# Kernel optimization log

Measured on AMD Instinct MI355X. Metric: run time of the kernel, lower is better.

Reference implementation:

```python
import jax, jax.numpy as jnp
import numpy as np

B, C, H, W = 8, 256, 128, 128
KC, VC, HEADS = 256, 256, 8


def setup_inputs() -> dict:
    key = jax.random.key(0)
    ks = jax.random.split(key, 10)
    s = 0.05
    return {
        "x": jax.random.normal(ks[0], (B, C, H, W), jnp.float32),
        "Wk": jax.random.normal(ks[1], (KC, C), jnp.float32) * s,
        "bk": jax.random.normal(ks[2], (KC,), jnp.float32) * s,
        "Wq": jax.random.normal(ks[3], (KC, C), jnp.float32) * s,
        "bq": jax.random.normal(ks[4], (KC,), jnp.float32) * s,
        "Wv": jax.random.normal(ks[5], (VC, C), jnp.float32) * s,
        "bv": jax.random.normal(ks[6], (VC,), jnp.float32) * s,
        "Wr": jax.random.normal(ks[7], (C, VC), jnp.float32) * s,
        "br": jax.random.normal(ks[8], (C,), jnp.float32) * s,
        "head_count": HEADS,
    }


def reference(x, Wk, bk, Wq, bq, Wv, bv, Wr, br, head_count):
    n, c, h, w = x.shape
    hw = h * w
    xf = x.reshape(n, c, hw)  # [n, C, S]
    # 1x1 convs == per-pixel linear projections
    keys = jnp.einsum('kc,ncs->nks', Wk, xf) + bk[None, :, None]
    queries = jnp.einsum('kc,ncs->nks', Wq, xf) + bq[None, :, None]
    values = jnp.einsum('vc,ncs->nvs', Wv, xf) + bv[None, :, None]

    dk = Wk.shape[0] // head_count
    dv = Wv.shape[0] // head_count
    # split heads along channel dim (matches torch channel slicing)
    K = jax.nn.softmax(keys.reshape(n, head_count, dk, hw), axis=-1)   # softmax over spatial
    Q = jax.nn.softmax(queries.reshape(n, head_count, dk, hw), axis=2) # softmax over key dim
    V = values.reshape(n, head_count, dv, hw)

    # context = K @ V^T : [n, h, dk, dv]
    ctx = jnp.einsum('nhks,nhvs->nhkv', K, V)
    # attended = ctx^T @ Q : [n, h, dv, S]
    att = jnp.einsum('nhkv,nhks->nhvs', ctx, Q).reshape(n, head_count * dv, h, w)

    attention = jnp.einsum('ov,nvhw->nohw', Wr, att) + br[None, :, None, None]
    # attention map: per-head mean over key dim, then mean over heads
    attention_map = K.mean(axis=2).mean(axis=1).reshape(n, h, w)
    # torch returns the LAST head's context (loop variable after the loop)
    context_last = ctx[:, -1]
    return attention, context_last, attention_map
```

## Files before the change

kernel.cpp:

```cpp
#include <hip/hip_runtime.h>
#include <hip/hip_bf16.h>

typedef float f32x4 __attribute__((ext_vector_type(4)));
typedef short s16x8 __attribute__((ext_vector_type(8)));
typedef __bf16 bf16x8 __attribute__((ext_vector_type(8)));
typedef unsigned short u16;

#define DEVI __device__ __forceinline__

static constexpr int    HW      = 16384;
static constexpr size_t BSTRIDE = (size_t)256 * HW;

static constexpr size_t oXBT   = 0;
static constexpr size_t oEK    = oXBT  + (size_t)8 * HW * 256 * 2;
static constexpr size_t oQT    = oEK   + (size_t)8 * 256 * HW * 2;
static constexpr size_t oVB    = oQT   + (size_t)8 * HW * 256 * 2;
static constexpr size_t oWK    = oVB   + (size_t)8 * 256 * HW * 2;
static constexpr size_t oBIAS  = oWK   + (size_t)768 * 256 * 2;
static constexpr size_t oISE   = oBIAS + 4096;
static constexpr size_t oPS    = oISE  + 8192;
static constexpr size_t oCTX   = oPS   + (size_t)256 * 2048 * 4;
static constexpr size_t oMB    = oCTX  + (size_t)64 * 1024 * 4;
static constexpr size_t oCPART = oMB   + (size_t)8 * 256 * 256 * 2;
static constexpr size_t oMPART = oCPART + (size_t)4096 * 1024 * 4;

DEVI float bf2f(short x) {
  unsigned u = ((unsigned)(unsigned short)x) << 16;
  return __builtin_bit_cast(float, u);
}
DEVI u16 f2bf(float x) { return __builtin_bit_cast(u16, (__bf16)x); }

DEVI void gld16(const void* g, void* l) {
  __builtin_amdgcn_global_load_lds(
      (__attribute__((address_space(1))) void*)(g),
      (__attribute__((address_space(3))) void*)(l), 16, 0, 0);
}

__global__ __launch_bounds__(256) void k_prep(
    const float* __restrict__ Wk, const float* __restrict__ Wq, const float* __restrict__ Wv,
    const float* __restrict__ bk, const float* __restrict__ bq, const float* __restrict__ bv,
    u16* __restrict__ Wkqv, float* __restrict__ bias)
{
  int i = blockIdx.x * 256 + threadIdx.x;
  for (int p = i; p < 768 * 256; p += 64 * 256) {
    float v = (p < 65536) ? Wk[p] : (p < 131072 ? Wq[p - 65536] : Wv[p - 131072]);
    Wkqv[p] = f2bf(v);
  }
  if (i < 768) bias[i] = (i < 256) ? bk[i] : (i < 512 ? bq[i - 256] : bv[i - 512]);
}

__global__ __launch_bounds__(256) void k_transpose(const float* __restrict__ in_, u16* __restrict__ out)
{
  __shared__ u16 lds[64 * 256];
  const int t = threadIdx.x;
  const int n = blockIdx.y;
  const int s0 = blockIdx.x * 64;
  const float* src = in_ + ((size_t)n * 256 + t) * HW + s0;
  #pragma unroll
  for (int i = 0; i < 16; ++i) {
    f32x4 v = *(const f32x4*)(src + i * 4);
    #pragma unroll
    for (int j = 0; j < 4; ++j) lds[(i * 4 + j) * 256 + t] = f2bf(v[j]);
  }
  __syncthreads();
  s16x8* gp = (s16x8*)(out + (size_t)n * BSTRIDE + (size_t)s0 * 256);
  const s16x8* lp = (const s16x8*)lds;
  #pragma unroll
  for (int i = 0; i < 8; ++i) gp[t + i * 256] = lp[t + i * 256];
}

__global__ __launch_bounds__(256) void k_proj(
    const u16* __restrict__ W, const u16* __restrict__ xbT, const float* __restrict__ bias,
    u16* __restrict__ ek, u16* __restrict__ qT, u16* __restrict__ vb, float* __restrict__ ps)
{
  __shared__ u16 smem[17408];
  u16* Al = smem;
  u16* Bl = smem + 8192;
  const int t = threadIdx.x;
  const int L = blockIdx.x;
  const int n  = L & 7;
  const int idx = L >> 3;
  const int mb = idx % 6;
  const int sb = idx / 6;
  const int m0 = mb * 128, s0 = sb * 128;
  const int lane = t & 63;
  const int l15 = lane & 15, l4 = lane >> 4;
  const int wv = t >> 6;
  const int wm = (wv & 1) * 64, wn = (wv >> 1) * 64;
  const u16* Ab = W + (size_t)m0 * 256;
  const u16* Bb = xbT + (size_t)n * BSTRIDE + (size_t)s0 * 256;
  const int ar = t >> 2, ac = (t & 3) * 8;

  f32x4 acc[4][4] = {};

  auto stage = [&](int buf, int k0) {
    gld16(Ab + (size_t)ar * 256 + k0 + ac,        Al + buf * 4096 + t * 8);
    gld16(Ab + (size_t)(ar + 64) * 256 + k0 + ac, Al + buf * 4096 + 2048 + t * 8);
    gld16(Bb + (size_t)ar * 256 + k0 + ac,        Bl + buf * 4096 + t * 8);
    gld16(Bb + (size_t)(ar + 64) * 256 + k0 + ac, Bl + buf * 4096 + 2048 + t * 8);
  };

  stage(0, 0);
  __syncthreads();
  #pragma unroll
  for (int kt = 0; kt < 8; ++kt) {
    const int buf = kt & 1;
    if (kt < 7) stage(buf ^ 1, (kt + 1) * 32);
    bf16x8 af[4], bff[4];
    #pragma unroll
    for (int g = 0; g < 4; ++g) {
      af[g]  = *(const bf16x8*)&Al[buf * 4096 + (wm + g * 16 + l15) * 32 + l4 * 8];
      bff[g] = *(const bf16x8*)&Bl[buf * 4096 + (wn + g * 16 + l15) * 32 + l4 * 8];
    }
    #pragma unroll
    for (int mg = 0; mg < 4; ++mg)
      #pragma unroll
      for (int ng = 0; ng < 4; ++ng)
        acc[mg][ng] = __builtin_amdgcn_mfma_f32_16x16x32_bf16(af[mg], bff[ng], acc[mg][ng], 0, 0, 0);
    __syncthreads();
  }

  #pragma unroll
  for (int mg = 0; mg < 4; ++mg)
    #pragma unroll
    for (int r = 0; r < 4; ++r) {
      const float bb = bias[m0 + wm + mg * 16 + l4 * 4 + r];
      #pragma unroll
      for (int ng = 0; ng < 4; ++ng) acc[mg][ng][r] += bb;
    }

  const int rowBase = (mb & 1) * 128;

  if (mb < 2) {
    #pragma unroll
    for (int mg = 0; mg < 4; ++mg)
      #pragma unroll
      for (int r = 0; r < 4; ++r) {
        float s_ = 0.f;
        #pragma unroll
        for (int ng = 0; ng < 4; ++ng) {
          const float e = __expf(acc[mg][ng][r]);
          acc[mg][ng][r] = e; s_ += e;
        }
        s_ += __shfl_xor(s_, 1); s_ += __shfl_xor(s_, 2);
        s_ += __shfl_xor(s_, 4); s_ += __shfl_xor(s_, 8);
        if (l15 == 0) {
          const int row = rowBase + wm + mg * 16 + l4 * 4 + r;
          ps[((size_t)(sb * 2 + (wn >> 6))) * 2048 + n * 256 + row] = s_;
        }
      }
    u16* O = ek + (size_t)n * BSTRIDE;
    #pragma unroll
    for (int mg = 0; mg < 4; ++mg)
      #pragma unroll
      for (int r = 0; r < 4; ++r) {
        const size_t row = rowBase + wm + mg * 16 + l4 * 4 + r;
        u16* op = O + row * HW + s0 + wn + l15;
        #pragma unroll
        for (int ng = 0; ng < 4; ++ng) op[ng * 16] = f2bf(acc[mg][ng][r]);
      }
  } else if (mb < 4) {
    #pragma unroll
    for (int hh = 0; hh < 2; ++hh)
      #pragma unroll
      for (int ng = 0; ng < 4; ++ng) {
        float s = 0.f;
        #pragma unroll
        for (int mg = hh * 2; mg < hh * 2 + 2; ++mg)
          #pragma unroll
          for (int r = 0; r < 4; ++r) { const float e = __expf(acc[mg][ng][r]); acc[mg][ng][r] = e; s += e; }
        s += __shfl_xor(s, 16);
        s += __shfl_xor(s, 32);
        const float inv = 1.f / s;
        #pragma unroll
        for (int mg = hh * 2; mg < hh * 2 + 2; ++mg)
          #pragma unroll
          for (int r = 0; r < 4; ++r) acc[mg][ng][r] *= inv;
      }
    #pragma unroll
    for (int mg = 0; mg < 4; ++mg)
      #pragma unroll
      for (int ng = 0; ng < 4; ++ng)
        #pragma unroll
        for (int r = 0; r < 4; ++r) {
          const int srow = wn + ng * 16 + l15;
          const int mcol = wm + mg * 16 + l4 * 4 + r;
          smem[srow * 136 + mcol] = f2bf(acc[mg][ng][r]);
        }
    __syncthreads();
    u16* O = qT + (size_t)n * BSTRIDE + (size_t)s0 * 256 + rowBase;
    #pragma unroll
    for (int it = 0; it < 8; ++it) {
      const int row = it * 16 + (t >> 4);
      *(s16x8*)(O + (size_t)row * 256 + (t & 15) * 8) = *(const s16x8*)&smem[row * 136 + (t & 15) * 8];
    }
  } else {
    u16* O = vb + (size_t)n * BSTRIDE;
    #pragma unroll
    for (int mg = 0; mg < 4; ++mg)
      #pragma unroll
      for (int r = 0; r < 4; ++r) {
        const size_t row = rowBase + wm + mg * 16 + l4 * 4 + r;
        u16* op = O + row * HW + s0 + wn + l15;
        #pragma unroll
        for (int ng = 0; ng < 4; ++ng) op[ng * 16] = f2bf(acc[mg][ng][r]);
      }
  }
}

__global__ __launch_bounds__(256) void k_inv(const float* __restrict__ ps, float* __restrict__ ise)
{
  const int i = blockIdx.x * 256 + threadIdx.x;
  float s = 0.f;
  for (int b = 0; b < 256; ++b) s += ps[(size_t)b * 2048 + i];
  ise[i] = 1.f / s;
}

__global__ __launch_bounds__(64) void k_ctx_part(
    const u16* __restrict__ ek, const u16* __restrict__ vb, const float* __restrict__ ise,
    float* __restrict__ cpart, float* __restrict__ mpart)
{
  const int blk = blockIdx.x;
  const int chunk = blk & 63, nh = blk >> 6;
  const int h = nh & 7, n = nh >> 3;
  const int lane = threadIdx.x;
  const int l15 = lane & 15, l4 = lane >> 4;
  const u16* kb = ek + ((size_t)n * 256 + h * 32) * HW;
  const u16* vv = vb + ((size_t)n * 256 + h * 32) * HW;
  const float iv0 = ise[n * 256 + h * 32 + l15];
  const float iv1 = ise[n * 256 + h * 32 + 16 + l15];
  f32x4 acc[2][2] = {};
  float macc[8][8] = {};
  const int sbase = chunk * 256 + l4 * 8;
  #pragma unroll
  for (int ks = 0; ks < 8; ++ks) {
    const int sb = sbase + ks * 32;
    bf16x8 ef[2], vf[2];
    #pragma unroll
    for (int g = 0; g < 2; ++g) {
      ef[g] = *(const bf16x8*)(kb + (size_t)(g * 16 + l15) * HW + sb);
      vf[g] = *(const bf16x8*)(vv + (size_t)(g * 16 + l15) * HW + sb);
    }
    #pragma unroll
    for (int j = 0; j < 8; ++j)
      macc[ks][j] = fmaf(iv0, (float)ef[0][j], fmaf(iv1, (float)ef[1][j], macc[ks][j]));
    #pragma unroll
    for (int a = 0; a < 2; ++a)
      #pragma unroll
      for (int b = 0; b < 2; ++b)
        acc[a][b] = __builtin_amdgcn_mfma_f32_16x16x32_bf16(ef[a], vf[b], acc[a][b], 0, 0, 0);
  }
  float* op = cpart + (size_t)blk * 1024;
  #pragma unroll
  for (int a = 0; a < 2; ++a)
    #pragma unroll
    for (int b = 0; b < 2; ++b)
      #pragma unroll
      for (int r = 0; r < 4; ++r)
        op[(a * 16 + l4 * 4 + r) * 32 + b * 16 + l15] = acc[a][b][r];
  #pragma unroll
  for (int ks = 0; ks < 8; ++ks)
    #pragma unroll
    for (int j = 0; j < 8; ++j) {
      float v = macc[ks][j];
      v += __shfl_xor(v, 1); v += __shfl_xor(v, 2);
      v += __shfl_xor(v, 4); v += __shfl_xor(v, 8);
      macc[ks][j] = v;
    }
  if (l15 == 0) {
    float* mp = mpart + ((size_t)h * 8 + n) * HW + sbase;
    #pragma unroll
    for (int ks = 0; ks < 8; ++ks) {
      f32x4 a = {macc[ks][0], macc[ks][1], macc[ks][2], macc[ks][3]};
      f32x4 b = {macc[ks][4], macc[ks][5], macc[ks][6], macc[ks][7]};
      *(f32x4*)(mp + ks * 32)     = a;
      *(f32x4*)(mp + ks * 32 + 4) = b;
    }
  }
}

__global__ __launch_bounds__(256) void k_ctx_reduce(
    const float* __restrict__ cpart, const float* __restrict__ ise,
    float* __restrict__ ctx, float* __restrict__ dctx)
{
  const int nh = blockIdx.x, n = nh >> 3, h = nh & 7, t = threadIdx.x;
  f32x4 a = {};
  for (int c = 0; c < 64; ++c) a += *(const f32x4*)(cpart + ((size_t)nh * 64 + c) * 1024 + t * 4);
  const float inv = ise[n * 256 + h * 32 + (t >> 3)];
  a *= inv;
  *(f32x4*)(ctx + (size_t)nh * 1024 + t * 4) = a;
  if (h == 7) *(f32x4*)(dctx + (size_t)n * 1024 + t * 4) = a;
}

__global__ __launch_bounds__(256) void k_mmat(
    const float* __restrict__ ctx, const float* __restrict__ Wr, u16* __restrict__ Mb)
{
  const int nh = blockIdx.x, n = nh >> 3, h = nh & 7, o = threadIdx.x;
  __shared__ float cl[1024];
  #pragma unroll
  for (int i = 0; i < 4; ++i) cl[o + i * 256] = ctx[(size_t)nh * 1024 + o + i * 256];
  __syncthreads();
  float wr[32];
  const float* wp = Wr + (size_t)o * 256 + h * 32;
  #pragma unroll
  for (int v = 0; v < 32; ++v) wr[v] = wp[v];
  u16* mp = Mb + ((size_t)n * 256 + o) * 256 + h * 32;
  #pragma unroll 4
  for (int k = 0; k < 32; ++k) {
    float s = 0.f;
    #pragma unroll
    for (int v = 0; v < 32; ++v) s += wr[v] * cl[k * 32 + v];
    mp[k] = f2bf(s);
  }
}

__global__ __launch_bounds__(256) void k_map_reduce(const float* __restrict__ mpart, float* __restrict__ dmap)
{
  const int i = blockIdx.x * 256 + threadIdx.x;
  f32x4 a = {};
  #pragma unroll
  for (int h = 0; h < 8; ++h) a += *(const f32x4*)(mpart + (size_t)h * 131072 + (size_t)i * 4);
  a *= (1.0f / 256.0f);
  *(f32x4*)(dmap + (size_t)i * 4) = a;
}

__global__ __launch_bounds__(256) void k_attn(
    const u16* __restrict__ Mb, const u16* __restrict__ qT, const float* __restrict__ br,
    float* __restrict__ Out)
{
  __shared__ u16 Al[2][4096];
  __shared__ u16 Bl[2][4096];
  const int t = threadIdx.x;
  const int L = blockIdx.x;
  const int n = L & 7;
  const int idx = L >> 3;
  const int m0 = (idx & 1) * 128;
  const int s0 = (idx >> 1) * 128;
  const int lane = t & 63;
  const int l15 = lane & 15, l4 = lane >> 4;
  const int wv = t >> 6;
  const int wm = (wv & 1) * 64, wn = (wv >> 1) * 64;
  const u16* Ab = Mb + (size_t)n * 65536 + (size_t)m0 * 256;
  const u16* Bb = qT + (size_t)n * BSTRIDE + (size_t)s0 * 256;
  const int ar = t >> 2, ac = (t & 3) * 8;

  f32x4 acc[4][4] = {};

  auto stage = [&](int buf, int k0) {
    gld16(Ab + (size_t)ar * 256 + k0 + ac,        &Al[buf][t * 8]);
    gld16(Ab + (size_t)(ar + 64) * 256 + k0 + ac, &Al[buf][2048 + t * 8]);
    gld16(Bb + (size_t)ar * 256 + k0 + ac,        &Bl[buf][t * 8]);
    gld16(Bb + (size_t)(ar + 64) * 256 + k0 + ac, &Bl[buf][2048 + t * 8]);
  };

  stage(0, 0);
  __syncthreads();
  #pragma unroll
  for (int kt = 0; kt < 8; ++kt) {
    const int buf = kt & 1;
    if (kt < 7) stage(buf ^ 1, (kt + 1) * 32);
    bf16x8 af[4], bff[4];
    #pragma unroll
    for (int g = 0; g < 4; ++g) {
      af[g]  = *(const bf16x8*)&Al[buf][(wm + g * 16 + l15) * 32 + l4 * 8];
      bff[g] = *(const bf16x8*)&Bl[buf][(wn + g * 16 + l15) * 32 + l4 * 8];
    }
    #pragma unroll
    for (int mg = 0; mg < 4; ++mg)
      #pragma unroll
      for (int ng = 0; ng < 4; ++ng)
        acc[mg][ng] = __builtin_amdgcn_mfma_f32_16x16x32_bf16(af[mg], bff[ng], acc[mg][ng], 0, 0, 0);
    __syncthreads();
  }

  float* O = Out + (size_t)n * BSTRIDE;
  #pragma unroll
  for (int mg = 0; mg < 4; ++mg)
    #pragma unroll
    for (int r = 0; r < 4; ++r) {
      const size_t row = m0 + wm + mg * 16 + l4 * 4 + r;
      const float bb = br[row];
      float* op = O + row * HW + s0 + wn + l15;
      #pragma unroll
      for (int ng = 0; ng < 4; ++ng) op[ng * 16] = acc[mg][ng][r] + bb;
    }
}

extern "C" void kernel_launch(void* const* d_in, const int* in_sizes, int n_in,
                              void* d_out, int out_size, void* d_ws, size_t ws_size,
                              hipStream_t stream)
{
  (void)in_sizes; (void)n_in; (void)out_size; (void)ws_size;
  const float* x  = (const float*)d_in[0];
  const float* Wk = (const float*)d_in[1];
  const float* bk = (const float*)d_in[2];
  const float* Wq = (const float*)d_in[3];
  const float* bq = (const float*)d_in[4];
  const float* Wv = (const float*)d_in[5];
  const float* bv = (const float*)d_in[6];
  const float* Wr = (const float*)d_in[7];
  const float* br = (const float*)d_in[8];

  char* ws = (char*)d_ws;
  u16*   xbT  = (u16*)(ws + oXBT);
  u16*   ek   = (u16*)(ws + oEK);
  u16*   qT   = (u16*)(ws + oQT);
  u16*   vb   = (u16*)(ws + oVB);
  u16*   Wkqv = (u16*)(ws + oWK);
  float* bias = (float*)(ws + oBIAS);
  float* ise  = (float*)(ws + oISE);
  float* ps   = (float*)(ws + oPS);
  float* ctx  = (float*)(ws + oCTX);
  u16*   Mb   = (u16*)(ws + oMB);
  float* cpart= (float*)(ws + oCPART);
  float* mpart= (float*)(ws + oMPART);

  float* attn = (float*)d_out;
  float* dctx = (float*)d_out + 33554432;
  float* dmap = (float*)d_out + 33562624;

  k_prep<<<64, 256, 0, stream>>>(Wk, Wq, Wv, bk, bq, bv, Wkqv, bias);
  k_transpose<<<dim3(256, 8), 256, 0, stream>>>(x, xbT);
  k_proj<<<6144, 256, 0, stream>>>(Wkqv, xbT, bias, ek, qT, vb, ps);
  k_inv<<<8, 256, 0, stream>>>(ps, ise);
  k_ctx_part<<<4096, 64, 0, stream>>>(ek, vb, ise, cpart, mpart);
  k_ctx_reduce<<<64, 256, 0, stream>>>(cpart, ise, ctx, dctx);
  k_mmat<<<64, 256, 0, stream>>>(ctx, Wr, Mb);
  k_map_reduce<<<128, 256, 0, stream>>>(mpart, dmap);
  k_attn<<<2048, 256, 0, stream>>>(Mb, qT, br, attn);
}
```

Measured before the change: 289.7 us.

## Split projection into K/V and Q kernels, load operands directly, vectorize stores

Splits the fused projection kernel into a K/V kernel and a separate Q kernel. All projection and output GEMMs now read MFMA operands straight from global memory instead of staging them through LDS with global_load_lds, and launch bounds ask for 3 blocks per CU. The K/V and attention kernels swap the MFMA operand order so each lane holds 4 consecutive spatial outputs, which allows vectorized 8-byte bf16 stores and 16-byte fp32 stores instead of scattered 2- and 4-byte stores. The risk is extra global/L2 traffic and latency from dropping LDS reuse and double buffering.

```diff
diff --git a/kernel.cpp b/kernel.cpp
--- a/kernel.cpp
+++ b/kernel.cpp
@@ -3,6 +3,7 @@
 
 typedef float f32x4 __attribute__((ext_vector_type(4)));
 typedef short s16x8 __attribute__((ext_vector_type(8)));
+typedef short s16x4 __attribute__((ext_vector_type(4)));
 typedef __bf16 bf16x8 __attribute__((ext_vector_type(8)));
 typedef unsigned short u16;
 
@@ -30,12 +31,6 @@
 }
 DEVI u16 f2bf(float x) { return __builtin_bit_cast(u16, (__bf16)x); }
 
-DEVI void gld16(const void* g, void* l) {
-  __builtin_amdgcn_global_load_lds(
-      (__attribute__((address_space(1))) void*)(g),
-      (__attribute__((address_space(3))) void*)(l), 16, 0, 0);
-}
-
 __global__ __launch_bounds__(256) void k_prep(
     const float* __restrict__ Wk, const float* __restrict__ Wq, const float* __restrict__ Wv,
     const float* __restrict__ bk, const float* __restrict__ bq, const float* __restrict__ bv,
@@ -69,55 +64,121 @@
   for (int i = 0; i < 8; ++i) gp[t + i * 256] = lp[t + i * 256];
 }
 
-__global__ __launch_bounds__(256) void k_proj(
+
+__global__ __launch_bounds__(256, 3) void k_projKV(
     const u16* __restrict__ W, const u16* __restrict__ xbT, const float* __restrict__ bias,
-    u16* __restrict__ ek, u16* __restrict__ qT, u16* __restrict__ vb, float* __restrict__ ps)
+    u16* __restrict__ ek, u16* __restrict__ vb, float* __restrict__ ps)
+{
+  const int t = threadIdx.x;
+  const int L = blockIdx.x;
+  const int n = L & 7;
+  const int idx = L >> 3;
+  const int mbi = idx & 3;
+  const int sb  = idx >> 2;
+  const bool isK = (mbi < 2);
+  const int m0 = (mbi & 1) * 128;
+  const int aBase = (isK ? 0 : 512) + m0;
+  const int s0 = sb * 128;
+  const int lane = t & 63;
+  const int l15 = lane & 15, l4 = (lane >> 4) & 3;
+  const int wv = t >> 6;
+  const int wm = (wv & 1) * 64, wn = (wv >> 1) * 64;
+
+  const u16* Ab = W + (size_t)aBase * 256;
+  const u16* Bb = xbT + (size_t)n * BSTRIDE + (size_t)s0 * 256;
+
+  float biasv[4];
+  #pragma unroll
+  for (int mf = 0; mf < 4; ++mf) biasv[mf] = bias[aBase + wm + mf * 16 + l15];
+
+  f32x4 acc[4][4] = {};
+  #pragma unroll
+  for (int kt = 0; kt < 8; ++kt) {
+    const int k0 = kt * 32 + l4 * 8;
+    bf16x8 af[4], bf[4];
+    #pragma unroll
+    for (int g = 0; g < 4; ++g) {
+      af[g] = *(const bf16x8*)(Ab + (size_t)(wm + g * 16 + l15) * 256 + k0);
+      bf[g] = *(const bf16x8*)(Bb + (size_t)(wn + g * 16 + l15) * 256 + k0);
+    }
+    #pragma unroll
+    for (int sf = 0; sf < 4; ++sf)
+      #pragma unroll
+      for (int mf = 0; mf < 4; ++mf)
+        acc[sf][mf] = __builtin_amdgcn_mfma_f32_16x16x32_bf16(bf[sf], af[mf], acc[sf][mf], 0, 0, 0);
+  }
+
+  u16* outb = (isK ? ek : vb) + (size_t)n * BSTRIDE;
+  if (isK) {
+    float rs[4] = {0.f, 0.f, 0.f, 0.f};
+    #pragma unroll
+    for (int sf = 0; sf < 4; ++sf)
+      #pragma unroll
+      for (int mf = 0; mf < 4; ++mf) {
+        s16x4 pk;
+        #pragma unroll
+        for (int r = 0; r < 4; ++r) {
+          const float e = __expf(acc[sf][mf][r] + biasv[mf]);
+          rs[mf] += e;
+          pk[r] = (short)f2bf(e);
+        }
+        *(s16x4*)(outb + (size_t)(m0 + wm + mf * 16 + l15) * HW + s0 + wn + sf * 16 + l4 * 4) = pk;
+      }
+    #pragma unroll
+    for (int mf = 0; mf < 4; ++mf) {
+      float v = rs[mf];
+      v += __shfl_xor(v, 16); v += __shfl_xor(v, 32);
+      if (l4 == 0)
+        ps[((size_t)(sb * 2 + (wn >> 6))) * 2048 + n * 256 + m0 + wm + mf * 16 + l15] = v;
+    }
+  } else {
+    #pragma unroll
+    for (int sf = 0; sf < 4; ++sf)
+      #pragma unroll
+      for (int mf = 0; mf < 4; ++mf) {
+        s16x4 pk;
+        #pragma unroll
+        for (int r = 0; r < 4; ++r) pk[r] = (short)f2bf(acc[sf][mf][r] + biasv[mf]);
+        *(s16x4*)(outb + (size_t)(m0 + wm + mf * 16 + l15) * HW + s0 + wn + sf * 16 + l4 * 4) = pk;
+      }
+  }
+}
+
+__global__ __launch_bounds__(256, 3) void k_projQ(
+    const u16* __restrict__ W, const u16* __restrict__ xbT, const float* __restrict__ bias,
+    u16* __restrict__ qT)
 {
   __shared__ u16 smem[17408];
-  u16* Al = smem;
-  u16* Bl = smem + 8192;
   const int t = threadIdx.x;
   const int L = blockIdx.x;
   const int n  = L & 7;
   const int idx = L >> 3;
-  const int mb = idx % 6;
-  const int sb = idx / 6;
-  const int m0 = mb * 128, s0 = sb * 128;
+  const int mbq = idx & 1;
+  const int sb  = idx >> 1;
+  const int m0 = 256 + mbq * 128, s0 = sb * 128;
   const int lane = t & 63;
-  const int l15 = lane & 15, l4 = lane >> 4;
+  const int l15 = lane & 15, l4 = (lane >> 4) & 3;
   const int wv = t >> 6;
   const int wm = (wv & 1) * 64, wn = (wv >> 1) * 64;
+
   const u16* Ab = W + (size_t)m0 * 256;
   const u16* Bb = xbT + (size_t)n * BSTRIDE + (size_t)s0 * 256;
-  const int ar = t >> 2, ac = (t & 3) * 8;
 
   f32x4 acc[4][4] = {};
-
-  auto stage = [&](int buf, int k0) {
-    gld16(Ab + (size_t)ar * 256 + k0 + ac,        Al + buf * 4096 + t * 8);
-    gld16(Ab + (size_t)(ar + 64) * 256 + k0 + ac, Al + buf * 4096 + 2048 + t * 8);
-    gld16(Bb + (size_t)ar * 256 + k0 + ac,        Bl + buf * 4096 + t * 8);
-    gld16(Bb + (size_t)(ar + 64) * 256 + k0 + ac, Bl + buf * 4096 + 2048 + t * 8);
-  };
-
-  stage(0, 0);
-  __syncthreads();
   #pragma unroll
   for (int kt = 0; kt < 8; ++kt) {
-    const int buf = kt & 1;
-    if (kt < 7) stage(buf ^ 1, (kt + 1) * 32);
-    bf16x8 af[4], bff[4];
+    const int k0 = kt * 32 + l4 * 8;
+    bf16x8 af[4], bf[4];
     #pragma unroll
     for (int g = 0; g < 4; ++g) {
-      af[g]  = *(const bf16x8*)&Al[buf * 4096 + (wm + g * 16 + l15) * 32 + l4 * 8];
-      bff[g] = *(const bf16x8*)&Bl[buf * 4096 + (wn + g * 16 + l15) * 32 + l4 * 8];
+      af[g] = *(const bf16x8*)(Ab + (size_t)(wm + g * 16 + l15) * 256 + k0);
+      bf[g] = *(const bf16x8*)(Bb + (size_t)(wn + g * 16 + l15) * 256 + k0);
     }
     #pragma unroll
     for (int mg = 0; mg < 4; ++mg)
       #pragma unroll
       for (int ng = 0; ng < 4; ++ng)
-        acc[mg][ng] = __builtin_amdgcn_mfma_f32_16x16x32_bf16(af[mg], bff[ng], acc[mg][ng], 0, 0, 0);
-    __syncthreads();
+        acc[mg][ng] = __builtin_amdgcn_mfma_f32_16x16x32_bf16(af[mg], bf[ng], acc[mg][ng], 0, 0, 0);
   }
 
   #pragma unroll
@@ -129,83 +190,92 @@
       for (int ng = 0; ng < 4; ++ng) acc[mg][ng][r] += bb;
     }
 
-  const int rowBase = (mb & 1) * 128;
-
-  if (mb < 2) {
-    #pragma unroll
-    for (int mg = 0; mg < 4; ++mg)
+  #pragma unroll
+  for (int hh = 0; hh < 2; ++hh)
+    #pragma unroll
+    for (int ng = 0; ng < 4; ++ng) {
+      float s = 0.f;
+      #pragma unroll
+      for (int mg = hh * 2; mg < hh * 2 + 2; ++mg)
+        #pragma unroll
+        for (int r = 0; r < 4; ++r) { const float e = __expf(acc[mg][ng][r]); acc[mg][ng][r] = e; s += e; }
+      s += __shfl_xor(s, 16);
+      s += __shfl_xor(s, 32);
+      const float inv = 1.f / s;
+      #pragma unroll
+      for (int mg = hh * 2; mg < hh * 2 + 2; ++mg)
+        #pragma unroll
+        for (int r = 0; r < 4; ++r) acc[mg][ng][r] *= inv;
+    }
+  __syncthreads();
+  #pragma unroll
+  for (int mg = 0; mg < 4; ++mg)
+    #pragma unroll
+    for (int ng = 0; ng < 4; ++ng)
       #pragma unroll
       for (int r = 0; r < 4; ++r) {
-        float s_ = 0.f;
-        #pragma unroll
-        for (int ng = 0; ng < 4; ++ng) {
-          const float e = __expf(acc[mg][ng][r]);
-          acc[mg][ng][r] = e; s_ += e;
-        }
-        s_ += __shfl_xor(s_, 1); s_ += __shfl_xor(s_, 2);
-        s_ += __shfl_xor(s_, 4); s_ += __shfl_xor(s_, 8);
-        if (l15 == 0) {
-          const int row = rowBase + wm + mg * 16 + l4 * 4 + r;
-          ps[((size_t)(sb * 2 + (wn >> 6))) * 2048 + n * 256 + row] = s_;
-        }
+        const int srow = wn + ng * 16 + l15;
+        const int mcol = wm + mg * 16 + l4 * 4 + r;
+        smem[srow * 136 + mcol] = f2bf(acc[mg][ng][r]);
       }
-    u16* O = ek + (size_t)n * BSTRIDE;
-    #pragma unroll
-    for (int mg = 0; mg < 4; ++mg)
-      #pragma unroll
-      for (int r = 0; r < 4; ++r) {
-        const size_t row = rowBase + wm + mg * 16 + l4 * 4 + r;
-        u16* op = O + row * HW + s0 + wn + l15;
-        #pragma unroll
-        for (int ng = 0; ng < 4; ++ng) op[ng * 16] = f2bf(acc[mg][ng][r]);
-      }
-  } else if (mb < 4) {
-    #pragma unroll
-    for (int hh = 0; hh < 2; ++hh)
-      #pragma unroll
-      for (int ng = 0; ng < 4; ++ng) {
-        float s = 0.f;
-        #pragma unroll
-        for (int mg = hh * 2; mg < hh * 2 + 2; ++mg)
-          #pragma unroll
-          for (int r = 0; r < 4; ++r) { const float e = __expf(acc[mg][ng][r]); acc[mg][ng][r] = e; s += e; }
-        s += __shfl_xor(s, 16);
-        s += __shfl_xor(s, 32);
-        const float inv = 1.f / s;
-        #pragma unroll
-        for (int mg = hh * 2; mg < hh * 2 + 2; ++mg)
-          #pragma unroll
-          for (int r = 0; r < 4; ++r) acc[mg][ng][r] *= inv;
-      }
-    #pragma unroll
-    for (int mg = 0; mg < 4; ++mg)
-      #pragma unroll
-      for (int ng = 0; ng < 4; ++ng)
-        #pragma unroll
-        for (int r = 0; r < 4; ++r) {
-          const int srow = wn + ng * 16 + l15;
-          const int mcol = wm + mg * 16 + l4 * 4 + r;
-          smem[srow * 136 + mcol] = f2bf(acc[mg][ng][r]);
-        }
-    __syncthreads();
-    u16* O = qT + (size_t)n * BSTRIDE + (size_t)s0 * 256 + rowBase;
-    #pragma unroll
-    for (int it = 0; it < 8; ++it) {
-      const int row = it * 16 + (t >> 4);
-      *(s16x8*)(O + (size_t)row * 256 + (t & 15) * 8) = *(const s16x8*)&smem[row * 136 + (t & 15) * 8];
-    }
-  } else {
-    u16* O = vb + (size_t)n * BSTRIDE;
-    #pragma unroll
-    for (int mg = 0; mg < 4; ++mg)
-      #pragma unroll
-      for (int r = 0; r < 4; ++r) {
-        const size_t row = rowBase + wm + mg * 16 + l4 * 4 + r;
-        u16* op = O + row * HW + s0 + wn + l15;
-        #pragma unroll
-        for (int ng = 0; ng < 4; ++ng) op[ng * 16] = f2bf(acc[mg][ng][r]);
-      }
-  }
+  __syncthreads();
+  u16* O = qT + (size_t)n * BSTRIDE + (size_t)s0 * 256 + mbq * 128;
+  #pragma unroll
+  for (int it = 0; it < 8; ++it) {
+    const int row = it * 16 + (t >> 4);
+    *(s16x8*)(O + (size_t)row * 256 + (t & 15) * 8) = *(const s16x8*)&smem[row * 136 + (t & 15) * 8];
+  }
+}
+
+__global__ __launch_bounds__(256, 3) void k_attn2(
+    const u16* __restrict__ Mb, const u16* __restrict__ qT, const float* __restrict__ br,
+    float* __restrict__ Out)
+{
+  const int t = threadIdx.x;
+  const int L = blockIdx.x;
+  const int n = L & 7;
+  const int idx = L >> 3;
+  const int mb = idx & 1;
+  const int sb = idx >> 1;
+  const int m0 = mb * 128;
+  const int s0 = sb * 128;
+  const int lane = t & 63;
+  const int l15 = lane & 15, l4 = (lane >> 4) & 3;
+  const int wv = t >> 6;
+  const int wm = (wv & 1) * 64, wn = (wv >> 1) * 64;
+
+  const u16* Ab = Mb + (size_t)n * 65536 + (size_t)m0 * 256;
+  const u16* Bb = qT + (size_t)n * BSTRIDE + (size_t)s0 * 256;
+
+  float biasv[4];
+  #pragma unroll
+  for (int mf = 0; mf < 4; ++mf) biasv[mf] = br[m0 + wm + mf * 16 + l15];
+
+  f32x4 acc[4][4] = {};
+  #pragma unroll
+  for (int kt = 0; kt < 8; ++kt) {
+    const int k0 = kt * 32 + l4 * 8;
+    bf16x8 af[4], bf[4];
+    #pragma unroll
+    for (int g = 0; g < 4; ++g) {
+      af[g] = *(const bf16x8*)(Ab + (size_t)(wm + g * 16 + l15) * 256 + k0);
+      bf[g] = *(const bf16x8*)(Bb + (size_t)(wn + g * 16 + l15) * 256 + k0);
+    }
+    #pragma unroll
+    for (int sf = 0; sf < 4; ++sf)
+      #pragma unroll
+      for (int mf = 0; mf < 4; ++mf)
+        acc[sf][mf] = __builtin_amdgcn_mfma_f32_16x16x32_bf16(bf[sf], af[mf], acc[sf][mf], 0, 0, 0);
+  }
+
+  float* ob = Out + (size_t)n * BSTRIDE;
+  #pragma unroll
+  for (int sf = 0; sf < 4; ++sf)
+    #pragma unroll
+    for (int mf = 0; mf < 4; ++mf) {
+      f32x4 o = acc[sf][mf] + biasv[mf];
+      *(f32x4*)(ob + (size_t)(m0 + wm + mf * 16 + l15) * HW + s0 + wn + sf * 16 + l4 * 4) = o;
+    }
 }
 
 __global__ __launch_bounds__(256) void k_inv(const float* __restrict__ ps, float* __restrict__ ise)
@@ -322,68 +392,6 @@
   for (int h = 0; h < 8; ++h) a += *(const f32x4*)(mpart + (size_t)h * 131072 + (size_t)i * 4);
   a *= (1.0f / 256.0f);
   *(f32x4*)(dmap + (size_t)i * 4) = a;
-}
-
-__global__ __launch_bounds__(256) void k_attn(
-    const u16* __restrict__ Mb, const u16* __restrict__ qT, const float* __restrict__ br,
-    float* __restrict__ Out)
-{
-  __shared__ u16 Al[2][4096];
-  __shared__ u16 Bl[2][4096];
-  const int t = threadIdx.x;
-  const int L = blockIdx.x;
-  const int n = L & 7;
-  const int idx = L >> 3;
-  const int m0 = (idx & 1) * 128;
-  const int s0 = (idx >> 1) * 128;
-  const int lane = t & 63;
-  const int l15 = lane & 15, l4 = lane >> 4;
-  const int wv = t >> 6;
-  const int wm = (wv & 1) * 64, wn = (wv >> 1) * 64;
-  const u16* Ab = Mb + (size_t)n * 65536 + (size_t)m0 * 256;
-  const u16* Bb = qT + (size_t)n * BSTRIDE + (size_t)s0 * 256;
-  const int ar = t >> 2, ac = (t & 3) * 8;
-
-  f32x4 acc[4][4] = {};
-
-  auto stage = [&](int buf, int k0) {
-    gld16(Ab + (size_t)ar * 256 + k0 + ac,        &Al[buf][t * 8]);
-    gld16(Ab + (size_t)(ar + 64) * 256 + k0 + ac, &Al[buf][2048 + t * 8]);
-    gld16(Bb + (size_t)ar * 256 + k0 + ac,        &Bl[buf][t * 8]);
-    gld16(Bb + (size_t)(ar + 64) * 256 + k0 + ac, &Bl[buf][2048 + t * 8]);
-  };
-
-  stage(0, 0);
-  __syncthreads();
-  #pragma unroll
-  for (int kt = 0; kt < 8; ++kt) {
-    const int buf = kt & 1;
-    if (kt < 7) stage(buf ^ 1, (kt + 1) * 32);
-    bf16x8 af[4], bff[4];
-    #pragma unroll
-    for (int g = 0; g < 4; ++g) {
-      af[g]  = *(const bf16x8*)&Al[buf][(wm + g * 16 + l15) * 32 + l4 * 8];
-      bff[g] = *(const bf16x8*)&Bl[buf][(wn + g * 16 + l15) * 32 + l4 * 8];
-    }
-    #pragma unroll
-    for (int mg = 0; mg < 4; ++mg)
-      #pragma unroll
-      for (int ng = 0; ng < 4; ++ng)
-        acc[mg][ng] = __builtin_amdgcn_mfma_f32_16x16x32_bf16(af[mg], bff[ng], acc[mg][ng], 0, 0, 0);
-    __syncthreads();
-  }
-
-  float* O = Out + (size_t)n * BSTRIDE;
-  #pragma unroll
-  for (int mg = 0; mg < 4; ++mg)
-    #pragma unroll
-    for (int r = 0; r < 4; ++r) {
-      const size_t row = m0 + wm + mg * 16 + l4 * 4 + r;
-      const float bb = br[row];
-      float* op = O + row * HW + s0 + wn + l15;
-      #pragma unroll
-      for (int ng = 0; ng < 4; ++ng) op[ng * 16] = acc[mg][ng][r] + bb;
-    }
 }
 
 extern "C" void kernel_launch(void* const* d_in, const int* in_sizes, int n_in,
@@ -421,11 +429,12 @@
 
   k_prep<<<64, 256, 0, stream>>>(Wk, Wq, Wv, bk, bq, bv, Wkqv, bias);
   k_transpose<<<dim3(256, 8), 256, 0, stream>>>(x, xbT);
-  k_proj<<<6144, 256, 0, stream>>>(Wkqv, xbT, bias, ek, qT, vb, ps);
+  k_projKV<<<4096, 256, 0, stream>>>(Wkqv, xbT, bias, ek, vb, ps);
   k_inv<<<8, 256, 0, stream>>>(ps, ise);
+  k_projQ<<<2048, 256, 0, stream>>>(Wkqv, xbT, bias, qT);
   k_ctx_part<<<4096, 64, 0, stream>>>(ek, vb, ise, cpart, mpart);
   k_ctx_reduce<<<64, 256, 0, stream>>>(cpart, ise, ctx, dctx);
   k_mmat<<<64, 256, 0, stream>>>(ctx, Wr, Mb);
   k_map_reduce<<<128, 256, 0, stream>>>(mpart, dmap);
-  k_attn<<<2048, 256, 0, stream>>>(Mb, qT, br, attn);
-}
+  k_attn2<<<2048, 256, 0, stream>>>(Mb, qT, br, attn);
+}
```

Result: slower. 442.2 us (+52.6%).
